# Performance work log

Hardware: AMD Instinct MI355X
Metric: run time of the kernel (lower is better)

The kernel has to match this reference:

```python
import jax, jax.numpy as jnp
import numpy as np

B, Q, KV, D, H = 16, 32, 4096, 1024, 16
DH = D // H  # 64


def setup_inputs() -> dict:
    key = jax.random.key(0)
    ks = jax.random.split(key, 10)
    s = 0.02
    return {
        "x": jax.random.normal(ks[0], (B, Q, D), dtype=jnp.float32),
        "cache_k": jax.random.normal(ks[1], (B, KV, D), dtype=jnp.float32),
        "cache_v": jax.random.normal(ks[2], (B, KV, D), dtype=jnp.float32),
        "Wq": jax.random.normal(ks[3], (D, D), dtype=jnp.float32) * s,
        "bq": jnp.zeros((D,), dtype=jnp.float32),
        "Wk": jax.random.normal(ks[4], (D, D), dtype=jnp.float32) * s,
        "Wv": jax.random.normal(ks[5], (D, D), dtype=jnp.float32) * s,
        "bv": jnp.zeros((D,), dtype=jnp.float32),
        "Wo": jax.random.normal(ks[6], (D, D), dtype=jnp.float32) * s,
        "bo": jnp.zeros((D,), dtype=jnp.float32),
    }


def reference(x, cache_k, cache_v, Wq, bq, Wk, Wv, bv, Wo, bo):
    # Projections (self-attention decode step; key Linear has no bias in source)
    q = x @ Wq + bq                                   # [B, Q, D]
    curr_k = x @ Wk                                   # [B, Q, D]
    curr_v = x @ Wv + bv                              # [B, Q, D]
    # Concat-grown KV cache
    k = jnp.concatenate([cache_k, curr_k], axis=1)    # [B, KV+Q, D]
    v = jnp.concatenate([cache_v, curr_v], axis=1)    # [B, KV+Q, D]
    # Split heads; scale applied to q and k separately as (head_dim)**-0.25
    scale = DH ** (-0.25)
    qh = q.reshape(B, Q, H, DH) * scale               # [B, Q, H, DH]
    kh = k.reshape(B, KV + Q, H, DH) * scale          # [B, S, H, DH]
    vh = v.reshape(B, KV + Q, H, DH)                  # [B, S, H, DH]
    qk = jnp.einsum("bqhd,bshd->bhqs", qh, kh)        # [B, H, Q, S]
    w = jax.nn.softmax(qk, axis=-1)
    wv = jnp.einsum("bhqs,bshd->bqhd", w, vh).reshape(B, Q, D)
    return wv @ Wo + bo                               # [B, Q, D]
```

## Files before the change

### kernel.cpp

```cpp
#include <hip/hip_runtime.h>
#include <hip/hip_bf16.h>

#define BATCH 16
#define QLEN 32
#define KVLEN 4096
#define DMODEL 1024
#define NHEAD 16
#define DHEAD 64

typedef short bf16x8 __attribute__((ext_vector_type(8)));
typedef float f32x4 __attribute__((ext_vector_type(4)));

__device__ __forceinline__ unsigned short f2bf(float f) {
    unsigned int u = __float_as_uint(f);
    unsigned int r = (u + 0x7fffu + ((u >> 16) & 1u)) >> 16;
    return (unsigned short)r;
}

__device__ __forceinline__ unsigned int pack2(float a, float b) {
    return (unsigned int)f2bf(a) | ((unsigned int)f2bf(b) << 16);
}

__device__ __forceinline__ bf16x8 cvt8(float4 a, float4 b) {
    bf16x8 t;
    t[0] = (short)f2bf(a.x); t[1] = (short)f2bf(a.y);
    t[2] = (short)f2bf(a.z); t[3] = (short)f2bf(a.w);
    t[4] = (short)f2bf(b.x); t[5] = (short)f2bf(b.y);
    t[6] = (short)f2bf(b.z); t[7] = (short)f2bf(b.w);
    return t;
}

template <bool HAS_BIAS>
__device__ void gemm_body(const float* __restrict__ A, const float* __restrict__ W,
                          const float* __restrict__ bias, float* __restrict__ out,
                          int m0, int ncol, short* As, short* WT) {
    const int tid = threadIdx.x;
    const int l = tid & 63, w = tid >> 6;
    const int x = l & 15, g = l >> 4;
    const int wm = w >> 1, wn = w & 1;

    f32x4 acc[4][2] = {};

    for (int ko = 0; ko < 32; ++ko) {
#pragma unroll
        for (int c = 0; c < 4; ++c) {
            int e = tid * 4 + c * 1024;
            int row = e >> 5, col = e & 31;
            float4 v = *reinterpret_cast<const float4*>(
                &A[(size_t)(m0 + row) * DMODEL + ko * 32 + col]);
            short4 s4 = make_short4((short)f2bf(v.x), (short)f2bf(v.y),
                                    (short)f2bf(v.z), (short)f2bf(v.w));
            *reinterpret_cast<short4*>(&As[row * 40 + col]) = s4;
        }
#pragma unroll
        for (int c = 0; c < 2; ++c) {
            int e = tid * 4 + c * 1024;
            int kr = e >> 6, nc = e & 63;
            float4 v = *reinterpret_cast<const float4*>(
                &W[(size_t)(ko * 32 + kr) * DMODEL + ncol + nc]);
            WT[(nc + 0) * 40 + kr] = (short)f2bf(v.x);
            WT[(nc + 1) * 40 + kr] = (short)f2bf(v.y);
            WT[(nc + 2) * 40 + kr] = (short)f2bf(v.z);
            WT[(nc + 3) * 40 + kr] = (short)f2bf(v.w);
        }
        __syncthreads();

        bf16x8 af[4], bf[2];
#pragma unroll
        for (int mi = 0; mi < 4; ++mi)
            af[mi] = *reinterpret_cast<const bf16x8*>(
                &As[(wm * 64 + mi * 16 + x) * 40 + g * 8]);
#pragma unroll
        for (int nj = 0; nj < 2; ++nj)
            bf[nj] = *reinterpret_cast<const bf16x8*>(
                &WT[(wn * 32 + nj * 16 + x) * 40 + g * 8]);
#pragma unroll
        for (int mi = 0; mi < 4; ++mi)
#pragma unroll
            for (int nj = 0; nj < 2; ++nj)
                acc[mi][nj] = __builtin_amdgcn_mfma_f32_16x16x32_bf16(
                    af[mi], bf[nj], acc[mi][nj], 0, 0, 0);
        __syncthreads();
    }

#pragma unroll
    for (int nj = 0; nj < 2; ++nj) {
        int gcol = ncol + wn * 32 + nj * 16 + x;
        float bv = 0.0f;
        if (HAS_BIAS) bv = bias[gcol];
#pragma unroll
        for (int mi = 0; mi < 4; ++mi) {
#pragma unroll
            for (int r = 0; r < 4; ++r) {
                int grow = m0 + wm * 64 + mi * 16 + g * 4 + r;
                out[(size_t)grow * DMODEL + gcol] = acc[mi][nj][r] + bv;
            }
        }
    }
}

__global__ __launch_bounds__(256) void proj_kernel(
    const float* __restrict__ x, const float* __restrict__ Wq,
    const float* __restrict__ bq, const float* __restrict__ Wk,
    const float* __restrict__ Wv, const float* __restrict__ bv,
    float* __restrict__ q_ws, float* __restrict__ k_ws, float* __restrict__ v_ws) {
    __shared__ short As[128 * 40];
    __shared__ short WT[64 * 40];
    int m0 = blockIdx.x * 128;
    int grp = blockIdx.y >> 4;
    int ncol = (blockIdx.y & 15) * 64;
    if (grp == 0)      gemm_body<true >(x, Wq, bq,      q_ws, m0, ncol, As, WT);
    else if (grp == 1) gemm_body<false>(x, Wk, nullptr, k_ws, m0, ncol, As, WT);
    else               gemm_body<true >(x, Wv, bv,      v_ws, m0, ncol, As, WT);
}

__global__ __launch_bounds__(256) void outproj_kernel(
    const float* __restrict__ wv, const float* __restrict__ Wo,
    const float* __restrict__ bo, float* __restrict__ out) {
    __shared__ short As[128 * 40];
    __shared__ short WT[64 * 40];
    gemm_body<true>(wv, Wo, bo, out, blockIdx.x * 128, blockIdx.y * 64, As, WT);
}

__global__ __launch_bounds__(256, 1) void attn_kernel(
    const float* __restrict__ cache_k, const float* __restrict__ cache_v,
    const float* __restrict__ q_ws, const float* __restrict__ k_ws,
    const float* __restrict__ v_ws, float* __restrict__ wv_ws) {
    __shared__ unsigned short Plds[4][32][72];
    __shared__ float Olds[4][32][68];
    __shared__ float red_m[4][2][16];
    __shared__ float red_l[4][2][16];

    const int bid = blockIdx.x;
    const int b = bid >> 4, h = bid & 15;
    const int tid = threadIdx.x;
    const int l = tid & 63, w = tid >> 6;
    const int x = l & 15, g = l >> 4;

    bf16x8 qf[2][2];
#pragma unroll
    for (int qg = 0; qg < 2; ++qg) {
#pragma unroll
        for (int kg = 0; kg < 2; ++kg) {
            const float* qp = &q_ws[(size_t)(b * QLEN + qg * 16 + x) * DMODEL +
                                    h * DHEAD + kg * 32 + g * 8];
            float4 v0 = *reinterpret_cast<const float4*>(qp);
            float4 v1 = *reinterpret_cast<const float4*>(qp + 4);
            const float s = 0.125f;
            float4 a = make_float4(v0.x * s, v0.y * s, v0.z * s, v0.w * s);
            float4 c2 = make_float4(v1.x * s, v1.y * s, v1.z * s, v1.w * s);
            qf[kg][qg] = cvt8(a, c2);
        }
    }

    float m_run[2] = {-1e30f, -1e30f};
    float l_run[2] = {0.0f, 0.0f};
    f32x4 Oacc[4][2] = {};

    for (int t = w; t < 65; t += 4) {
        const int s0 = t * 64;
        const bool cur = (t == 64);
        const float* Kb = cur ? &k_ws[(size_t)b * QLEN * DMODEL]
                              : &cache_k[(size_t)b * KVLEN * DMODEL];
        const float* Vb = cur ? &v_ws[(size_t)b * QLEN * DMODEL]
                              : &cache_v[(size_t)b * KVLEN * DMODEL];

        bf16x8 ka[4][2];
#pragma unroll
        for (int sg = 0; sg < 4; ++sg) {
            int srow = sg * 16 + x;
            srow = cur ? (srow > QLEN - 1 ? QLEN - 1 : srow) : (s0 + srow);
            const float* kp = &Kb[(size_t)srow * DMODEL + h * DHEAD + g * 8];
#pragma unroll
            for (int kg = 0; kg < 2; ++kg) {
                float4 v0 = *reinterpret_cast<const float4*>(kp + kg * 32);
                float4 v1 = *reinterpret_cast<const float4*>(kp + kg * 32 + 4);
                ka[sg][kg] = cvt8(v0, v1);
            }
        }

        f32x4 c[4][2] = {};
#pragma unroll
        for (int sg = 0; sg < 4; ++sg) {
#pragma unroll
            for (int qg = 0; qg < 2; ++qg) {
                c[sg][qg] = __builtin_amdgcn_mfma_f32_16x16x32_bf16(
                    ka[sg][0], qf[0][qg], c[sg][qg], 0, 0, 0);
                c[sg][qg] = __builtin_amdgcn_mfma_f32_16x16x32_bf16(
                    ka[sg][1], qf[1][qg], c[sg][qg], 0, 0, 0);
            }
        }
        if (cur) {
#pragma unroll
            for (int qg = 0; qg < 2; ++qg)
#pragma unroll
                for (int r = 0; r < 4; ++r) {
                    c[2][qg][r] = -1e30f;
                    c[3][qg][r] = -1e30f;
                }
        }

        float sc[2];
#pragma unroll
        for (int qg = 0; qg < 2; ++qg) {
            float mx = c[0][qg][0];
#pragma unroll
            for (int sg = 0; sg < 4; ++sg)
#pragma unroll
                for (int r = 0; r < 4; ++r) mx = fmaxf(mx, c[sg][qg][r]);
            mx = fmaxf(mx, __shfl_xor(mx, 16));
            mx = fmaxf(mx, __shfl_xor(mx, 32));
            float mn = fmaxf(m_run[qg], mx);
            sc[qg] = __expf(m_run[qg] - mn);
            m_run[qg] = mn;
            float rs = 0.0f;
#pragma unroll
            for (int sg = 0; sg < 4; ++sg)
#pragma unroll
                for (int r = 0; r < 4; ++r) {
                    float p = __expf(c[sg][qg][r] - mn);
                    c[sg][qg][r] = p;
                    rs += p;
                }
            rs += __shfl_xor(rs, 16);
            rs += __shfl_xor(rs, 32);
            l_run[qg] = l_run[qg] * sc[qg] + rs;
        }

#pragma unroll
        for (int dg = 0; dg < 4; ++dg)
#pragma unroll
            for (int qg = 0; qg < 2; ++qg)
#pragma unroll
                for (int r = 0; r < 4; ++r) Oacc[dg][qg][r] *= sc[qg];

#pragma unroll
        for (int sg = 0; sg < 4; ++sg)
#pragma unroll
            for (int qg = 0; qg < 2; ++qg) {
                unsigned int w0 = pack2(c[sg][qg][0], c[sg][qg][1]);
                unsigned int w1 = pack2(c[sg][qg][2], c[sg][qg][3]);
                unsigned short* p = &Plds[w][qg * 16 + x][sg * 16 + g * 4];
                *reinterpret_cast<unsigned int*>(p) = w0;
                *reinterpret_cast<unsigned int*>(p + 2) = w1;
            }
        bf16x8 pb[2][2];
#pragma unroll
        for (int kg = 0; kg < 2; ++kg)
#pragma unroll
            for (int qg = 0; qg < 2; ++qg)
                pb[kg][qg] = *reinterpret_cast<const bf16x8*>(
                    &Plds[w][qg * 16 + x][kg * 32 + g * 8]);

        bf16x8 va[4][2];
#pragma unroll
        for (int dg = 0; dg < 4; ++dg)
#pragma unroll
            for (int kg = 0; kg < 2; ++kg) {
                bf16x8 tt;
#pragma unroll
                for (int j = 0; j < 8; ++j) {
                    int sv = kg * 32 + g * 8 + j;
                    int srow = cur ? (sv > QLEN - 1 ? QLEN - 1 : sv) : (s0 + sv);
                    tt[j] = (short)f2bf(
                        Vb[(size_t)srow * DMODEL + h * DHEAD + dg * 16 + x]);
                }
                va[dg][kg] = tt;
            }

#pragma unroll
        for (int dg = 0; dg < 4; ++dg)
#pragma unroll
            for (int qg = 0; qg < 2; ++qg) {
                Oacc[dg][qg] = __builtin_amdgcn_mfma_f32_16x16x32_bf16(
                    va[dg][0], pb[0][qg], Oacc[dg][qg], 0, 0, 0);
                Oacc[dg][qg] = __builtin_amdgcn_mfma_f32_16x16x32_bf16(
                    va[dg][1], pb[1][qg], Oacc[dg][qg], 0, 0, 0);
            }
    }

    if (l < 16) {
#pragma unroll
        for (int qg = 0; qg < 2; ++qg) {
            red_m[w][qg][l] = m_run[qg];
            red_l[w][qg][l] = l_run[qg];
        }
    }
    __syncthreads();

    float cself[2];
#pragma unroll
    for (int qg = 0; qg < 2; ++qg) {
        float M = red_m[0][qg][x];
#pragma unroll
        for (int ww = 1; ww < 4; ++ww) M = fmaxf(M, red_m[ww][qg][x]);
        cself[qg] = __expf(m_run[qg] - M);
    }
#pragma unroll
    for (int dg = 0; dg < 4; ++dg)
#pragma unroll
        for (int qg = 0; qg < 2; ++qg) {
            f32x4 v = Oacc[dg][qg];
            v[0] *= cself[qg]; v[1] *= cself[qg];
            v[2] *= cself[qg]; v[3] *= cself[qg];
            *reinterpret_cast<f32x4*>(&Olds[w][qg * 16 + x][dg * 16 + g * 4]) = v;
        }
    __syncthreads();

    {
        int q = tid >> 3;
        int d0 = (tid & 7) * 8;
        int qg = q >> 4, xq = q & 15;
        float M = red_m[0][qg][xq];
#pragma unroll
        for (int ww = 1; ww < 4; ++ww) M = fmaxf(M, red_m[ww][qg][xq]);
        float L = 0.0f;
#pragma unroll
        for (int ww = 0; ww < 4; ++ww)
            L += __expf(red_m[ww][qg][xq] - M) * red_l[ww][qg][xq];
        float inv = 1.0f / L;
        float o[8] = {};
#pragma unroll
        for (int ww = 0; ww < 4; ++ww) {
            float4 a0 = *reinterpret_cast<const float4*>(&Olds[ww][q][d0]);
            float4 a1 = *reinterpret_cast<const float4*>(&Olds[ww][q][d0 + 4]);
            o[0] += a0.x; o[1] += a0.y; o[2] += a0.z; o[3] += a0.w;
            o[4] += a1.x; o[5] += a1.y; o[6] += a1.z; o[7] += a1.w;
        }
        float* op = &wv_ws[(size_t)(b * QLEN + q) * DMODEL + h * DHEAD + d0];
        float4 w0 = make_float4(o[0] * inv, o[1] * inv, o[2] * inv, o[3] * inv);
        float4 w1 = make_float4(o[4] * inv, o[5] * inv, o[6] * inv, o[7] * inv);
        *reinterpret_cast<float4*>(op) = w0;
        *reinterpret_cast<float4*>(op + 4) = w1;
    }
}

extern "C" void kernel_launch(void* const* d_in, const int* in_sizes, int n_in,
                              void* d_out, int out_size, void* d_ws, size_t ws_size,
                              hipStream_t stream) {
    (void)in_sizes; (void)n_in; (void)out_size; (void)ws_size;
    const float* x       = (const float*)d_in[0];
    const float* cache_k = (const float*)d_in[1];
    const float* cache_v = (const float*)d_in[2];
    const float* Wq      = (const float*)d_in[3];
    const float* bq      = (const float*)d_in[4];
    const float* Wk      = (const float*)d_in[5];
    const float* Wv      = (const float*)d_in[6];
    const float* bv      = (const float*)d_in[7];
    const float* Wo      = (const float*)d_in[8];
    const float* bo      = (const float*)d_in[9];
    float* out = (float*)d_out;

    float* ws    = (float*)d_ws;
    float* q_ws  = ws;
    float* k_ws  = ws + 1 * 512 * 1024;
    float* v_ws  = ws + 2 * 512 * 1024;
    float* wv_ws = ws + 3 * 512 * 1024;

    proj_kernel<<<dim3(4, 48), 256, 0, stream>>>(x, Wq, bq, Wk, Wv, bv,
                                                 q_ws, k_ws, v_ws);
    attn_kernel<<<dim3(256), 256, 0, stream>>>(cache_k, cache_v, q_ws, k_ws,
                                               v_ws, wv_ws);
    outproj_kernel<<<dim3(4, 16), 256, 0, stream>>>(wv_ws, Wo, bo, out);
}
```

Baseline: 705.3 us.

## Split attention over KV with merge kernel and pre-convert operands to bf16

```diff
diff --git a/kernel.cpp b/kernel.cpp
--- a/kernel.cpp
+++ b/kernel.cpp
@@ -30,158 +30,208 @@
     return t;
 }
 
-template <bool HAS_BIAS>
-__device__ void gemm_body(const float* __restrict__ A, const float* __restrict__ W,
-                          const float* __restrict__ bias, float* __restrict__ out,
-                          int m0, int ncol, short* As, short* WT) {
+__global__ __launch_bounds__(256) void convert_x_kernel(
+    const float* __restrict__ x, unsigned short* __restrict__ xb) {
+    int gidx = (blockIdx.x * 256 + threadIdx.x) * 8;
+    float4 a = *reinterpret_cast<const float4*>(&x[gidx]);
+    float4 b = *reinterpret_cast<const float4*>(&x[gidx + 4]);
+    *reinterpret_cast<bf16x8*>(&xb[gidx]) = cvt8(a, b);
+}
+
+__global__ __launch_bounds__(256) void transpose_w_kernel(
+    const float* __restrict__ Wq, const float* __restrict__ Wk,
+    const float* __restrict__ Wv, const float* __restrict__ Wo,
+    unsigned short* __restrict__ WT_all) {
+    __shared__ unsigned short T[64 * 72];
+    const int z = blockIdx.z;
+    const float* W = (z == 0) ? Wq : (z == 1) ? Wk : (z == 2) ? Wv : Wo;
+    unsigned short* WT = WT_all + (size_t)z * DMODEL * DMODEL;
+    const int n0 = blockIdx.x * 64, k0 = blockIdx.y * 64;
+    const int tid = threadIdx.x;
+    const int col4 = tid & 15, krow = tid >> 4;
+#pragma unroll
+    for (int p = 0; p < 4; ++p) {
+        int k = krow + p * 16;
+        float4 v = *reinterpret_cast<const float4*>(
+            &W[(size_t)(k0 + k) * DMODEL + n0 + col4 * 4]);
+        T[(col4 * 4 + 0) * 72 + k] = f2bf(v.x);
+        T[(col4 * 4 + 1) * 72 + k] = f2bf(v.y);
+        T[(col4 * 4 + 2) * 72 + k] = f2bf(v.z);
+        T[(col4 * 4 + 3) * 72 + k] = f2bf(v.w);
+    }
+    __syncthreads();
+    const int c8 = tid & 7;
+#pragma unroll
+    for (int p = 0; p < 2; ++p) {
+        int n = (tid >> 3) + p * 32;
+        bf16x8 v = *reinterpret_cast<const bf16x8*>(&T[n * 72 + c8 * 8]);
+        *reinterpret_cast<bf16x8*>(&WT[(size_t)(n0 + n) * DMODEL + k0 + c8 * 8]) = v;
+    }
+}
+
+template <bool HAS_BIAS, bool BF16_OUT>
+__device__ __forceinline__ void gemm_body(
+    const unsigned short* __restrict__ A, const unsigned short* __restrict__ BT,
+    const float* __restrict__ bias, float scale, void* __restrict__ outp,
+    int m0, int ncol, unsigned short* As, unsigned short* Bs) {
     const int tid = threadIdx.x;
     const int l = tid & 63, w = tid >> 6;
     const int x = l & 15, g = l >> 4;
     const int wm = w >> 1, wn = w & 1;
+    const int rowS = tid >> 3, colS = (tid & 7) * 8;
 
     f32x4 acc[4][2] = {};
 
-    for (int ko = 0; ko < 32; ++ko) {
+    for (int ko = 0; ko < 16; ++ko) {
 #pragma unroll
         for (int c = 0; c < 4; ++c) {
-            int e = tid * 4 + c * 1024;
-            int row = e >> 5, col = e & 31;
-            float4 v = *reinterpret_cast<const float4*>(
-                &A[(size_t)(m0 + row) * DMODEL + ko * 32 + col]);
-            short4 s4 = make_short4((short)f2bf(v.x), (short)f2bf(v.y),
-                                    (short)f2bf(v.z), (short)f2bf(v.w));
-            *reinterpret_cast<short4*>(&As[row * 40 + col]) = s4;
+            int row = rowS + c * 32;
+            bf16x8 v = *reinterpret_cast<const bf16x8*>(
+                &A[(size_t)(m0 + row) * DMODEL + ko * 64 + colS]);
+            *reinterpret_cast<bf16x8*>(&As[row * 72 + colS]) = v;
         }
 #pragma unroll
         for (int c = 0; c < 2; ++c) {
-            int e = tid * 4 + c * 1024;
-            int kr = e >> 6, nc = e & 63;
-            float4 v = *reinterpret_cast<const float4*>(
-                &W[(size_t)(ko * 32 + kr) * DMODEL + ncol + nc]);
-            WT[(nc + 0) * 40 + kr] = (short)f2bf(v.x);
-            WT[(nc + 1) * 40 + kr] = (short)f2bf(v.y);
-            WT[(nc + 2) * 40 + kr] = (short)f2bf(v.z);
-            WT[(nc + 3) * 40 + kr] = (short)f2bf(v.w);
+            int row = rowS + c * 32;
+            bf16x8 v = *reinterpret_cast<const bf16x8*>(
+                &BT[(size_t)(ncol + row) * DMODEL + ko * 64 + colS]);
+            *reinterpret_cast<bf16x8*>(&Bs[row * 72 + colS]) = v;
         }
         __syncthreads();
 
-        bf16x8 af[4], bf[2];
+        bf16x8 af[4][2], bfr[2][2];
 #pragma unroll
         for (int mi = 0; mi < 4; ++mi)
-            af[mi] = *reinterpret_cast<const bf16x8*>(
-                &As[(wm * 64 + mi * 16 + x) * 40 + g * 8]);
+#pragma unroll
+            for (int kk = 0; kk < 2; ++kk)
+                af[mi][kk] = *reinterpret_cast<const bf16x8*>(
+                    &As[(wm * 64 + mi * 16 + x) * 72 + kk * 32 + g * 8]);
 #pragma unroll
         for (int nj = 0; nj < 2; ++nj)
-            bf[nj] = *reinterpret_cast<const bf16x8*>(
-                &WT[(wn * 32 + nj * 16 + x) * 40 + g * 8]);
-#pragma unroll
-        for (int mi = 0; mi < 4; ++mi)
-#pragma unroll
-            for (int nj = 0; nj < 2; ++nj)
-                acc[mi][nj] = __builtin_amdgcn_mfma_f32_16x16x32_bf16(
-                    af[mi], bf[nj], acc[mi][nj], 0, 0, 0);
+#pragma unroll
+            for (int kk = 0; kk < 2; ++kk)
+                bfr[nj][kk] = *reinterpret_cast<const bf16x8*>(
+                    &Bs[(wn * 32 + nj * 16 + x) * 72 + kk * 32 + g * 8]);
+#pragma unroll
+        for (int kk = 0; kk < 2; ++kk)
+#pragma unroll
+            for (int mi = 0; mi < 4; ++mi)
+#pragma unroll
+                for (int nj = 0; nj < 2; ++nj)
+                    acc[mi][nj] = __builtin_amdgcn_mfma_f32_16x16x32_bf16(
+                        af[mi][kk], bfr[nj][kk], acc[mi][nj], 0, 0, 0);
         __syncthreads();
     }
 
 #pragma unroll
     for (int nj = 0; nj < 2; ++nj) {
         int gcol = ncol + wn * 32 + nj * 16 + x;
-        float bv = 0.0f;
-        if (HAS_BIAS) bv = bias[gcol];
+        float bv = HAS_BIAS ? bias[gcol] : 0.0f;
 #pragma unroll
         for (int mi = 0; mi < 4; ++mi) {
 #pragma unroll
             for (int r = 0; r < 4; ++r) {
                 int grow = m0 + wm * 64 + mi * 16 + g * 4 + r;
-                out[(size_t)grow * DMODEL + gcol] = acc[mi][nj][r] + bv;
-            }
-        }
-    }
-}
-
-__global__ __launch_bounds__(256) void proj_kernel(
-    const float* __restrict__ x, const float* __restrict__ Wq,
-    const float* __restrict__ bq, const float* __restrict__ Wk,
-    const float* __restrict__ Wv, const float* __restrict__ bv,
-    float* __restrict__ q_ws, float* __restrict__ k_ws, float* __restrict__ v_ws) {
-    __shared__ short As[128 * 40];
-    __shared__ short WT[64 * 40];
+                float v = (acc[mi][nj][r] + bv) * scale;
+                if (BF16_OUT)
+                    ((unsigned short*)outp)[(size_t)grow * DMODEL + gcol] = f2bf(v);
+                else
+                    ((float*)outp)[(size_t)grow * DMODEL + gcol] = v;
+            }
+        }
+    }
+}
+
+__global__ __launch_bounds__(256, 2) void proj_kernel(
+    const unsigned short* __restrict__ xb, const unsigned short* __restrict__ WTq,
+    const unsigned short* __restrict__ WTk, const unsigned short* __restrict__ WTv,
+    const float* __restrict__ bq, const float* __restrict__ bv,
+    unsigned short* __restrict__ qb, unsigned short* __restrict__ kb,
+    unsigned short* __restrict__ vb) {
+    __shared__ unsigned short As[128 * 72];
+    __shared__ unsigned short Bs[64 * 72];
     int m0 = blockIdx.x * 128;
     int grp = blockIdx.y >> 4;
     int ncol = (blockIdx.y & 15) * 64;
-    if (grp == 0)      gemm_body<true >(x, Wq, bq,      q_ws, m0, ncol, As, WT);
-    else if (grp == 1) gemm_body<false>(x, Wk, nullptr, k_ws, m0, ncol, As, WT);
-    else               gemm_body<true >(x, Wv, bv,      v_ws, m0, ncol, As, WT);
-}
-
-__global__ __launch_bounds__(256) void outproj_kernel(
-    const float* __restrict__ wv, const float* __restrict__ Wo,
+    if (grp == 0)
+        gemm_body<true, true>(xb, WTq, bq, 0.125f, qb, m0, ncol, As, Bs);
+    else if (grp == 1)
+        gemm_body<false, true>(xb, WTk, nullptr, 1.0f, kb, m0, ncol, As, Bs);
+    else
+        gemm_body<true, true>(xb, WTv, bv, 1.0f, vb, m0, ncol, As, Bs);
+}
+
+__global__ __launch_bounds__(256, 2) void outproj_kernel(
+    const unsigned short* __restrict__ wvb, const unsigned short* __restrict__ WTo,
     const float* __restrict__ bo, float* __restrict__ out) {
-    __shared__ short As[128 * 40];
-    __shared__ short WT[64 * 40];
-    gemm_body<true>(wv, Wo, bo, out, blockIdx.x * 128, blockIdx.y * 64, As, WT);
-}
-
-__global__ __launch_bounds__(256, 1) void attn_kernel(
+    __shared__ unsigned short As[128 * 72];
+    __shared__ unsigned short Bs[64 * 72];
+    gemm_body<true, false>(wvb, WTo, bo, 1.0f, out, blockIdx.x * 128,
+                           blockIdx.y * 64, As, Bs);
+}
+
+__global__ __launch_bounds__(256, 4) void attn_kernel(
     const float* __restrict__ cache_k, const float* __restrict__ cache_v,
-    const float* __restrict__ q_ws, const float* __restrict__ k_ws,
-    const float* __restrict__ v_ws, float* __restrict__ wv_ws) {
+    const unsigned short* __restrict__ qb, const unsigned short* __restrict__ kb,
+    const unsigned short* __restrict__ vb, float* __restrict__ pm,
+    float* __restrict__ pl, float* __restrict__ pO) {
     __shared__ unsigned short Plds[4][32][72];
-    __shared__ float Olds[4][32][68];
-    __shared__ float red_m[4][2][16];
-    __shared__ float red_l[4][2][16];
 
     const int bid = blockIdx.x;
     const int b = bid >> 4, h = bid & 15;
+    const int split = blockIdx.y;
     const int tid = threadIdx.x;
     const int l = tid & 63, w = tid >> 6;
     const int x = l & 15, g = l >> 4;
+    const int slice = split * 4 + w;
 
     bf16x8 qf[2][2];
 #pragma unroll
-    for (int qg = 0; qg < 2; ++qg) {
-#pragma unroll
-        for (int kg = 0; kg < 2; ++kg) {
-            const float* qp = &q_ws[(size_t)(b * QLEN + qg * 16 + x) * DMODEL +
-                                    h * DHEAD + kg * 32 + g * 8];
-            float4 v0 = *reinterpret_cast<const float4*>(qp);
-            float4 v1 = *reinterpret_cast<const float4*>(qp + 4);
-            const float s = 0.125f;
-            float4 a = make_float4(v0.x * s, v0.y * s, v0.z * s, v0.w * s);
-            float4 c2 = make_float4(v1.x * s, v1.y * s, v1.z * s, v1.w * s);
-            qf[kg][qg] = cvt8(a, c2);
-        }
-    }
+    for (int qg = 0; qg < 2; ++qg)
+#pragma unroll
+        for (int kg = 0; kg < 2; ++kg)
+            qf[kg][qg] = *reinterpret_cast<const bf16x8*>(
+                &qb[(size_t)(b * QLEN + qg * 16 + x) * DMODEL + h * DHEAD +
+                    kg * 32 + g * 8]);
 
     float m_run[2] = {-1e30f, -1e30f};
     float l_run[2] = {0.0f, 0.0f};
     f32x4 Oacc[4][2] = {};
 
-    for (int t = w; t < 65; t += 4) {
+    for (int t = slice; t < 65; t += 16) {
+        const bool cur = (t == 64);
         const int s0 = t * 64;
-        const bool cur = (t == 64);
-        const float* Kb = cur ? &k_ws[(size_t)b * QLEN * DMODEL]
-                              : &cache_k[(size_t)b * KVLEN * DMODEL];
-        const float* Vb = cur ? &v_ws[(size_t)b * QLEN * DMODEL]
-                              : &cache_v[(size_t)b * KVLEN * DMODEL];
 
         bf16x8 ka[4][2];
-#pragma unroll
-        for (int sg = 0; sg < 4; ++sg) {
-            int srow = sg * 16 + x;
-            srow = cur ? (srow > QLEN - 1 ? QLEN - 1 : srow) : (s0 + srow);
-            const float* kp = &Kb[(size_t)srow * DMODEL + h * DHEAD + g * 8];
-#pragma unroll
-            for (int kg = 0; kg < 2; ++kg) {
-                float4 v0 = *reinterpret_cast<const float4*>(kp + kg * 32);
-                float4 v1 = *reinterpret_cast<const float4*>(kp + kg * 32 + 4);
-                ka[sg][kg] = cvt8(v0, v1);
+        if (cur) {
+#pragma unroll
+            for (int sg = 0; sg < 4; ++sg) {
+                int srow = sg * 16 + x;
+                srow = srow > QLEN - 1 ? QLEN - 1 : srow;
+                const unsigned short* kp =
+                    &kb[(size_t)(b * QLEN + srow) * DMODEL + h * DHEAD + g * 8];
+#pragma unroll
+                for (int kg = 0; kg < 2; ++kg)
+                    ka[sg][kg] = *reinterpret_cast<const bf16x8*>(kp + kg * 32);
+            }
+        } else {
+            const float* Kb = &cache_k[(size_t)b * KVLEN * DMODEL];
+#pragma unroll
+            for (int sg = 0; sg < 4; ++sg) {
+                const float* kp = &Kb[(size_t)(s0 + sg * 16 + x) * DMODEL +
+                                      h * DHEAD + g * 8];
+#pragma unroll
+                for (int kg = 0; kg < 2; ++kg) {
+                    float4 v0 = *reinterpret_cast<const float4*>(kp + kg * 32);
+                    float4 v1 = *reinterpret_cast<const float4*>(kp + kg * 32 + 4);
+                    ka[sg][kg] = cvt8(v0, v1);
+                }
             }
         }
 
         f32x4 c[4][2] = {};
 #pragma unroll
-        for (int sg = 0; sg < 4; ++sg) {
+        for (int sg = 0; sg < 4; ++sg)
 #pragma unroll
             for (int qg = 0; qg < 2; ++qg) {
                 c[sg][qg] = __builtin_amdgcn_mfma_f32_16x16x32_bf16(
@@ -189,7 +239,6 @@
                 c[sg][qg] = __builtin_amdgcn_mfma_f32_16x16x32_bf16(
                     ka[sg][1], qf[1][qg], c[sg][qg], 0, 0, 0);
             }
-        }
         if (cur) {
 #pragma unroll
             for (int qg = 0; qg < 2; ++qg)
@@ -253,20 +302,37 @@
                     &Plds[w][qg * 16 + x][kg * 32 + g * 8]);
 
         bf16x8 va[4][2];
-#pragma unroll
-        for (int dg = 0; dg < 4; ++dg)
-#pragma unroll
-            for (int kg = 0; kg < 2; ++kg) {
-                bf16x8 tt;
-#pragma unroll
-                for (int j = 0; j < 8; ++j) {
-                    int sv = kg * 32 + g * 8 + j;
-                    int srow = cur ? (sv > QLEN - 1 ? QLEN - 1 : sv) : (s0 + sv);
-                    tt[j] = (short)f2bf(
-                        Vb[(size_t)srow * DMODEL + h * DHEAD + dg * 16 + x]);
+        if (cur) {
+#pragma unroll
+            for (int dg = 0; dg < 4; ++dg)
+#pragma unroll
+                for (int kg = 0; kg < 2; ++kg) {
+                    bf16x8 tt;
+#pragma unroll
+                    for (int j = 0; j < 8; ++j) {
+                        int sv = kg * 32 + g * 8 + j;
+                        int srow = sv > QLEN - 1 ? QLEN - 1 : sv;
+                        tt[j] = (short)vb[(size_t)(b * QLEN + srow) * DMODEL +
+                                          h * DHEAD + dg * 16 + x];
+                    }
+                    va[dg][kg] = tt;
                 }
-                va[dg][kg] = tt;
-            }
+        } else {
+            const float* Vb = &cache_v[(size_t)b * KVLEN * DMODEL];
+#pragma unroll
+            for (int dg = 0; dg < 4; ++dg)
+#pragma unroll
+                for (int kg = 0; kg < 2; ++kg) {
+                    bf16x8 tt;
+#pragma unroll
+                    for (int j = 0; j < 8; ++j) {
+                        int srow = s0 + kg * 32 + g * 8 + j;
+                        tt[j] = (short)f2bf(
+                            Vb[(size_t)srow * DMODEL + h * DHEAD + dg * 16 + x]);
+                    }
+                    va[dg][kg] = tt;
+                }
+        }
 
 #pragma unroll
         for (int dg = 0; dg < 4; ++dg)
@@ -279,59 +345,45 @@
             }
     }
 
-    if (l < 16) {
+    const int p = bid * 16 + slice;
+    if (g == 0) {
 #pragma unroll
         for (int qg = 0; qg < 2; ++qg) {
-            red_m[w][qg][l] = m_run[qg];
-            red_l[w][qg][l] = l_run[qg];
-        }
-    }
-    __syncthreads();
-
-    float cself[2];
-#pragma unroll
-    for (int qg = 0; qg < 2; ++qg) {
-        float M = red_m[0][qg][x];
-#pragma unroll
-        for (int ww = 1; ww < 4; ++ww) M = fmaxf(M, red_m[ww][qg][x]);
-        cself[qg] = __expf(m_run[qg] - M);
+            pm[p * 32 + qg * 16 + x] = m_run[qg];
+            pl[p * 32 + qg * 16 + x] = l_run[qg];
+        }
     }
 #pragma unroll
     for (int dg = 0; dg < 4; ++dg)
 #pragma unroll
-        for (int qg = 0; qg < 2; ++qg) {
-            f32x4 v = Oacc[dg][qg];
-            v[0] *= cself[qg]; v[1] *= cself[qg];
-            v[2] *= cself[qg]; v[3] *= cself[qg];
-            *reinterpret_cast<f32x4*>(&Olds[w][qg * 16 + x][dg * 16 + g * 4]) = v;
-        }
-    __syncthreads();
-
-    {
-        int q = tid >> 3;
-        int d0 = (tid & 7) * 8;
-        int qg = q >> 4, xq = q & 15;
-        float M = red_m[0][qg][xq];
-#pragma unroll
-        for (int ww = 1; ww < 4; ++ww) M = fmaxf(M, red_m[ww][qg][xq]);
-        float L = 0.0f;
-#pragma unroll
-        for (int ww = 0; ww < 4; ++ww)
-            L += __expf(red_m[ww][qg][xq] - M) * red_l[ww][qg][xq];
-        float inv = 1.0f / L;
-        float o[8] = {};
-#pragma unroll
-        for (int ww = 0; ww < 4; ++ww) {
-            float4 a0 = *reinterpret_cast<const float4*>(&Olds[ww][q][d0]);
-            float4 a1 = *reinterpret_cast<const float4*>(&Olds[ww][q][d0 + 4]);
-            o[0] += a0.x; o[1] += a0.y; o[2] += a0.z; o[3] += a0.w;
-            o[4] += a1.x; o[5] += a1.y; o[6] += a1.z; o[7] += a1.w;
-        }
-        float* op = &wv_ws[(size_t)(b * QLEN + q) * DMODEL + h * DHEAD + d0];
-        float4 w0 = make_float4(o[0] * inv, o[1] * inv, o[2] * inv, o[3] * inv);
-        float4 w1 = make_float4(o[4] * inv, o[5] * inv, o[6] * inv, o[7] * inv);
-        *reinterpret_cast<float4*>(op) = w0;
-        *reinterpret_cast<float4*>(op + 4) = w1;
+        for (int qg = 0; qg < 2; ++qg)
+            *reinterpret_cast<f32x4*>(
+                &pO[(size_t)(p * 32 + qg * 16 + x) * DHEAD + dg * 16 + g * 4]) =
+                Oacc[dg][qg];
+}
+
+__global__ __launch_bounds__(256, 4) void merge_kernel(
+    const float* __restrict__ pm, const float* __restrict__ pl,
+    const float* __restrict__ pO, unsigned short* __restrict__ wvb) {
+    const int w = threadIdx.x >> 6, d = threadIdx.x & 63;
+    const int gw = blockIdx.x * 4 + w;
+#pragma unroll
+    for (int i = 0; i < 4; ++i) {
+        int row = gw * 4 + i;
+        int bh = row >> 5, q = row & 31;
+        int base = bh * 16;
+        float M = -1e30f;
+#pragma unroll
+        for (int s = 0; s < 16; ++s) M = fmaxf(M, pm[(base + s) * 32 + q]);
+        float L = 0.0f, O = 0.0f;
+#pragma unroll
+        for (int s = 0; s < 16; ++s) {
+            float ws = __expf(pm[(base + s) * 32 + q] - M);
+            L += ws * pl[(base + s) * 32 + q];
+            O += ws * pO[(size_t)((base + s) * 32 + q) * DHEAD + d];
+        }
+        int b = bh >> 4, h = bh & 15;
+        wvb[(size_t)(b * QLEN + q) * DMODEL + h * DHEAD + d] = f2bf(O / L);
     }
 }
 
@@ -351,15 +403,27 @@
     const float* bo      = (const float*)d_in[9];
     float* out = (float*)d_out;
 
-    float* ws    = (float*)d_ws;
-    float* q_ws  = ws;
-    float* k_ws  = ws + 1 * 512 * 1024;
-    float* v_ws  = ws + 2 * 512 * 1024;
-    float* wv_ws = ws + 3 * 512 * 1024;
-
-    proj_kernel<<<dim3(4, 48), 256, 0, stream>>>(x, Wq, bq, Wk, Wv, bv,
-                                                 q_ws, k_ws, v_ws);
-    attn_kernel<<<dim3(256), 256, 0, stream>>>(cache_k, cache_v, q_ws, k_ws,
-                                               v_ws, wv_ws);
-    outproj_kernel<<<dim3(4, 16), 256, 0, stream>>>(wv_ws, Wo, bo, out);
-}
+    unsigned short* U   = (unsigned short*)d_ws;
+    unsigned short* xb  = U;
+    unsigned short* WTq = U + (1u << 19);
+    unsigned short* WTk = WTq + (1u << 20);
+    unsigned short* WTv = WTk + (1u << 20);
+    unsigned short* WTo = WTv + (1u << 20);
+    unsigned short* qb  = WTo + (1u << 20);
+    unsigned short* kb  = qb + (1u << 19);
+    unsigned short* vb  = kb + (1u << 19);
+    unsigned short* wvb = vb + (1u << 19);
+    float* F  = (float*)((char*)d_ws + (16u << 20));
+    float* pm = F;
+    float* pl = pm + 4096 * 32;
+    float* pO = pl + 4096 * 32;
+
+    convert_x_kernel<<<256, 256, 0, stream>>>(x, xb);
+    transpose_w_kernel<<<dim3(16, 16, 4), 256, 0, stream>>>(Wq, Wk, Wv, Wo, WTq);
+    proj_kernel<<<dim3(4, 48), 256, 0, stream>>>(xb, WTq, WTk, WTv, bq, bv,
+                                                 qb, kb, vb);
+    attn_kernel<<<dim3(256, 4), 256, 0, stream>>>(cache_k, cache_v, qb, kb, vb,
+                                                  pm, pl, pO);
+    merge_kernel<<<512, 256, 0, stream>>>(pm, pl, pO, wvb);
+    outproj_kernel<<<dim3(4, 16), 256, 0, stream>>>(wvb, WTo, bo, out);
+}
```

New measurement: 647.2 us. 8.2% less time.
